# Kernel tuning notes

Hardware: AMD Instinct MI355X
Metric: run time of the kernel (lower is better)

Reference implementation:

```python
import jax, jax.numpy as jnp
import numpy as np

DIM = 768
HEADS = 12

def setup_inputs() -> dict:
    key = jax.random.key(0)
    ks = jax.random.split(key, 5)
    x = jax.random.normal(ks[0], (8, 1024, DIM), dtype=jnp.float32)
    s = 1.0 / np.sqrt(DIM)
    W_qkv = jax.random.normal(ks[1], (DIM, 3 * DIM), dtype=jnp.float32) * s
    b_qkv = jax.random.normal(ks[2], (3 * DIM,), dtype=jnp.float32) * 0.01
    W_proj = jax.random.normal(ks[3], (DIM, DIM), dtype=jnp.float32) * s
    b_proj = jax.random.normal(ks[4], (DIM,), dtype=jnp.float32) * 0.01
    return {"x": x, "W_qkv": W_qkv, "b_qkv": b_qkv, "W_proj": W_proj, "b_proj": b_proj}

def reference(x, W_qkv, b_qkv, W_proj, b_proj):
    B, T, D = x.shape
    H = HEADS
    hd = D // H
    scale = hd ** -0.5
    qkv = x @ W_qkv + b_qkv                      # [B,T,3D]
    qkv = qkv.reshape(B, T, 3, H, hd)
    q, k, v = jnp.moveaxis(qkv, 2, 0)            # each [B,T,H,hd]
    q = jnp.transpose(q, (0, 2, 1, 3))           # [B,H,T,hd]
    k = jnp.transpose(k, (0, 2, 1, 3))
    v = jnp.transpose(v, (0, 2, 1, 3))
    attn = jnp.einsum('bhqd,bhkd->bhqk', q, k) * scale
    attn = jax.nn.softmax(attn, axis=-1)
    y = jnp.einsum('bhqk,bhkd->bhqd', attn, v)   # [B,H,T,hd]
    y = jnp.transpose(y, (0, 2, 1, 3)).reshape(B, T, D)
    return y @ W_proj + b_proj
```

## Files before the change

### kernel.cpp

```cpp
#include <hip/hip_runtime.h>

typedef unsigned short u16;
typedef __attribute__((ext_vector_type(8))) short short8;
typedef __attribute__((ext_vector_type(4))) short short4v;
typedef __attribute__((ext_vector_type(2))) int int2v;
typedef __attribute__((ext_vector_type(4))) float f32x4;

#define DIM   768
#define HEADS 12
#define HD    64
#define BATCH 8
#define SEQ   1024
#define MTOK  (BATCH*SEQ)
#define NQKV  (3*DIM)
#define KP    72
#define EPAD  66
#define PSZ   ((size_t)BATCH*HEADS*SEQ*HD)
#define SCQ   0.1803368801f

__device__ __forceinline__ u16 f2bf(float f) {
  unsigned x = __float_as_uint(f);
  x += 0x7fffu + ((x >> 16) & 1u);
  return (u16)(x >> 16);
}

__device__ __forceinline__ void gload16(const u16* g, u16* l) {
  __builtin_amdgcn_global_load_lds(
      (const __attribute__((address_space(1))) unsigned int*)g,
      (__attribute__((address_space(3))) unsigned int*)l, 16, 0, 0);
}

#define XBLK 6144
#define QTBLK 1728
__global__ void cvt_all_k(const float* __restrict__ x,
                          const float* __restrict__ Wqkv,
                          const float* __restrict__ Wproj,
                          u16* __restrict__ xb, u16* __restrict__ wqkvt,
                          u16* __restrict__ wprojt) {
  __shared__ u16 tile[32][33];
  const int blk = blockIdx.x;
  if (blk < XBLK) {
    const int i = blk * 256 + threadIdx.x;
    float4 f = ((const float4*)x)[i];
    short4v o;
    o.x = (short)f2bf(f.x); o.y = (short)f2bf(f.y);
    o.z = (short)f2bf(f.z); o.w = (short)f2bf(f.w);
    ((short4v*)xb)[i] = o;
    return;
  }
  const float* in; u16* out; int K, N, n0, k0;
  if (blk < XBLK + QTBLK) {
    const int t = blk - XBLK;
    in = Wqkv; out = wqkvt; K = DIM; N = NQKV;
    n0 = (t % (NQKV / 32)) * 32; k0 = (t / (NQKV / 32)) * 32;
  } else {
    const int t = blk - XBLK - QTBLK;
    in = Wproj; out = wprojt; K = DIM; N = DIM;
    n0 = (t % (DIM / 32)) * 32; k0 = (t / (DIM / 32)) * 32;
  }
  const int tx = threadIdx.x & 31, ty = threadIdx.x >> 5;
  #pragma unroll
  for (int i = 0; i < 32; i += 8)
    tile[ty + i][tx] = f2bf(in[(size_t)(k0 + ty + i) * N + n0 + tx]);
  __syncthreads();
  #pragma unroll
  for (int i = 0; i < 32; i += 8)
    out[(size_t)(n0 + ty + i) * K + k0 + tx] = tile[tx][ty + i];
}

__global__ __launch_bounds__(256)
void gemm_qkv(const u16* __restrict__ A, const u16* __restrict__ Bt,
              const float* __restrict__ bias, u16* __restrict__ qkv) {
  __shared__ __align__(16) u16 smem[8 * 128 * 32];
  const int w = threadIdx.x >> 6, lane = threadIdx.x & 63;
  const int l15 = lane & 15, quad = lane >> 4;
  const int b_ = blockIdx.x;
  const int xcd = b_ & 7, j = b_ >> 3;
  const int m0 = ((j & 7) * 8 + xcd) * 128;
  const int n0 = (j >> 3) * 128;
  const int wm = (w >> 1) * 64, wn = (w & 1) * 64;

  f32x4 acc[4][4] = {};

  const int ar = threadIdx.x >> 2, ak = (threadIdx.x & 3) * 8;
  const u16* ga = A  + (size_t)(m0 + ar) * DIM + ak;
  const u16* gb = Bt + (size_t)(n0 + ar) * DIM + ak;
  const int lo = threadIdx.x * 8;

  auto qstage = [&](int c, int k0) {
    u16* base = smem + c * 16384;
    #pragma unroll
    for (int t = 0; t < 2; ++t) {
      gload16(ga + (size_t)t * 64 * DIM + k0,      base + lo + t * 2048);
      gload16(ga + (size_t)t * 64 * DIM + k0 + 32, base + 4096  + lo + t * 2048);
      gload16(gb + (size_t)t * 64 * DIM + k0,      base + 8192  + lo + t * 2048);
      gload16(gb + (size_t)t * 64 * DIM + k0 + 32, base + 12288 + lo + t * 2048);
    }
  };

  qstage(0, 0);

  #pragma unroll
  for (int it = 0; it < 12; ++it) {
    const int cur = it & 1;
    if (it < 11) qstage(cur ^ 1, (it + 1) * 64);
    if (it < 11) asm volatile("s_waitcnt vmcnt(8)" ::: "memory");
    else         asm volatile("s_waitcnt vmcnt(0)" ::: "memory");
    __builtin_amdgcn_s_barrier();

    const u16* hb = smem + cur * 16384;
    short8 af[4][2], bfr[4][2];
    #pragma unroll
    for (int kh = 0; kh < 2; ++kh) {
      const u16* lAh = hb + kh * 4096;
      const u16* lBh = hb + 8192 + kh * 4096;
      #pragma unroll
      for (int mt = 0; mt < 4; ++mt)
        af[mt][kh] = *(const short8*)&lAh[(wm + mt * 16 + l15) * 32 + quad * 8];
      #pragma unroll
      for (int nt = 0; nt < 4; ++nt)
        bfr[nt][kh] = *(const short8*)&lBh[(wn + nt * 16 + l15) * 32 + quad * 8];
    }

    asm volatile("s_waitcnt lgkmcnt(0)" ::: "memory");
    __builtin_amdgcn_s_barrier();

    #pragma unroll
    for (int kh = 0; kh < 2; ++kh)
      #pragma unroll
      for (int mt = 0; mt < 4; ++mt)
        #pragma unroll
        for (int nt = 0; nt < 4; ++nt)
          acc[mt][nt] = __builtin_amdgcn_mfma_f32_16x16x32_bf16(af[mt][kh], bfr[nt][kh], acc[mt][nt], 0, 0, 0);
  }

  const int bb = m0 >> 10;
  const int tb0 = (m0 & 1023) + wm;
  const int nh = n0 + wn;
  const int part = nh / DIM, idx = nh - part * DIM;
  const int h = idx >> 6;

  float bnl[4];
  #pragma unroll
  for (int nt = 0; nt < 4; ++nt) bnl[nt] = bias[nh + nt * 16 + l15];

  if (part < 2) {
    u16* dstbase = qkv + part * PSZ + ((size_t)(bb * HEADS + h) * SEQ + tb0) * HD;
    const float qsc = (part == 0) ? SCQ : 1.0f;
    const int erow = lane >> 3, ec8 = (lane & 7) * 8;
    #pragma unroll
    for (int mt = 0; mt < 4; ++mt) {
      u16* ep = smem + w * (16 * EPAD) + (mt & 1) * (4 * 16 * EPAD);
      #pragma unroll
      for (int nt = 0; nt < 4; ++nt)
        #pragma unroll
        for (int r = 0; r < 4; ++r)
          ep[(quad * 4 + r) * EPAD + nt * 16 + l15] = f2bf((acc[mt][nt][r] + bnl[nt]) * qsc);
      #pragma unroll
      for (int j2 = 0; j2 < 2; ++j2) {
        const int trow = j2 * 8 + erow;
        short8 vrow = *(const short8*)&ep[trow * EPAD + ec8];
        *(short8*)(dstbase + (size_t)(mt * 16 + trow) * HD + ec8) = vrow;
      }
    }
  } else {
    u16* vrow0 = qkv + 2 * PSZ + (size_t)(bb * HEADS + h) * HD * SEQ;
    #pragma unroll
    for (int nt = 0; nt < 4; ++nt) {
      const int d = nt * 16 + l15;
      u16* trow = vrow0 + (size_t)d * SEQ + tb0 + quad * 4;
      #pragma unroll
      for (int mt = 0; mt < 4; ++mt) {
        short4v pv;
        pv.x = (short)f2bf(acc[mt][nt][0] + bnl[nt]);
        pv.y = (short)f2bf(acc[mt][nt][1] + bnl[nt]);
        pv.z = (short)f2bf(acc[mt][nt][2] + bnl[nt]);
        pv.w = (short)f2bf(acc[mt][nt][3] + bnl[nt]);
        *(short4v*)(trow + mt * 16) = pv;
      }
    }
  }
}

__global__ __launch_bounds__(256)
void gemm_proj(const u16* __restrict__ A, const u16* __restrict__ Bt,
               const float* __restrict__ bias, float* __restrict__ outF) {
  __shared__ __align__(16) u16 smem[8 * 128 * 32];
  const int w = threadIdx.x >> 6, lane = threadIdx.x & 63;
  const int l15 = lane & 15, quad = lane >> 4;
  const int b_ = blockIdx.x;
  const int xcd = b_ & 7, j = b_ >> 3;
  const int m0 = ((j & 7) * 8 + xcd) * 128;
  const int n0 = (j >> 3) * 128;
  const int wm = (w >> 1) * 64, wn = (w & 1) * 64;

  f32x4 acc[4][4] = {};

  const int ar = threadIdx.x >> 2, ak = (threadIdx.x & 3) * 8;
  const u16* ga = A  + (size_t)(m0 + ar) * DIM + ak;
  const u16* gb = Bt + (size_t)(n0 + ar) * DIM + ak;
  const int lo = threadIdx.x * 8;

  auto pstage = [&](int c, int k0) {
    u16* base = smem + c * 16384;
    #pragma unroll
    for (int t = 0; t < 2; ++t) {
      gload16(ga + (size_t)t * 64 * DIM + k0,      base + lo + t * 2048);
      gload16(ga + (size_t)t * 64 * DIM + k0 + 32, base + 4096  + lo + t * 2048);
      gload16(gb + (size_t)t * 64 * DIM + k0,      base + 8192  + lo + t * 2048);
      gload16(gb + (size_t)t * 64 * DIM + k0 + 32, base + 12288 + lo + t * 2048);
    }
  };

  pstage(0, 0);
  __syncthreads();

  #pragma unroll
  for (int it = 0; it < 12; ++it) {
    const int cur = it & 1;
    if (it < 11) pstage(cur ^ 1, (it + 1) * 64);
    const u16* hb = smem + cur * 16384;
    #pragma unroll
    for (int kh = 0; kh < 2; ++kh) {
      const u16* lAh = hb + kh * 4096;
      const u16* lBh = hb + 8192 + kh * 4096;
      short8 af[4], bfr[4];
      #pragma unroll
      for (int mt = 0; mt < 4; ++mt)
        af[mt] = *(const short8*)&lAh[(wm + mt * 16 + l15) * 32 + quad * 8];
      #pragma unroll
      for (int nt = 0; nt < 4; ++nt)
        bfr[nt] = *(const short8*)&lBh[(wn + nt * 16 + l15) * 32 + quad * 8];
      #pragma unroll
      for (int mt = 0; mt < 4; ++mt)
        #pragma unroll
        for (int nt = 0; nt < 4; ++nt)
          acc[mt][nt] = __builtin_amdgcn_mfma_f32_16x16x32_bf16(af[mt], bfr[nt], acc[mt][nt], 0, 0, 0);
    }
    __syncthreads();
  }

  #pragma unroll
  for (int nt = 0; nt < 4; ++nt) {
    const int n = n0 + wn + nt * 16 + l15;
    const float bn = bias[n];
    #pragma unroll
    for (int mt = 0; mt < 4; ++mt)
      #pragma unroll
      for (int r = 0; r < 4; ++r) {
        const int m = m0 + wm + mt * 16 + quad * 4 + r;
        outF[(size_t)m * DIM + n] = acc[mt][nt][r] + bn;
      }
  }
}

__global__ __launch_bounds__(512, 4)
void attn_k(const u16* __restrict__ qb, const u16* __restrict__ kb,
            const u16* __restrict__ vtb, u16* __restrict__ yb) {
  const int bh = blockIdx.x, qt = blockIdx.y;
  const int tid = threadIdx.x;
  const int w = tid >> 6, lane = tid & 63;
  const int l15 = lane & 15, quad = lane >> 4;
  const int rg = w & 3;
  const int kh = w >> 2;
  const int nt0 = kh * 2;

  __shared__ __align__(16) u16 smem[27648];
  u16* lK  = smem;
  u16* lV  = smem + 4608;
  u16* lPq = smem + 9216 + rg * 2304;
  u16* stg = smem + 18432 + rg * 2304;
  float* fo = (float*)smem;

  const u16* qrow = qb + ((size_t)bh * SEQ + qt * 128 + rg * 32 + l15) * HD;
  short8 aq[2][2];
  #pragma unroll
  for (int qg = 0; qg < 2; ++qg) {
    aq[qg][0] = *(const short8*)(qrow + (size_t)qg * 16 * HD + quad * 8);
    aq[qg][1] = *(const short8*)(qrow + (size_t)qg * 16 * HD + 32 + quad * 8);
  }

  f32x4 o[2][4] = {};
  f32x4 sum[2] = {};

  const u16* kcbase = kb + (size_t)bh * SEQ * HD;
  const u16* vbase  = vtb + (size_t)bh * HD * SEQ;

  const int srow = tid >> 3, scol = tid & 7;
  const int sofs = srow * KP + scol * 8;
  const u16* kg = kcbase + tid * 8;
  const u16* vg = vbase + (size_t)srow * SEQ + scol * 8;

  short8 pk = *(const short8*)kg;
  short8 pv = *(const short8*)vg;

  short8 ones;
  #pragma unroll
  for (int i = 0; i < 8; ++i) ones[i] = (short)0x3f80;

  for (int kc = 0; kc < 16; ++kc) {
    *(short8*)&lK[sofs] = pk;
    *(short8*)&lV[sofs] = pv;
    __syncthreads();

    const int kn = (kc < 15) ? kc + 1 : 15;
    pk = *(const short8*)(kg + (size_t)kn * 64 * HD);
    pv = *(const short8*)(vg + kn * 64);

    short8 akf[2][2];
    #pragma unroll
    for (int i = 0; i < 2; ++i) {
      const int key = (nt0 + i) * 16 + l15;
      akf[i][0] = *(const short8*)&lK[key * KP + quad * 8];
      akf[i][1] = *(const short8*)&lK[key * KP + 32 + quad * 8];
    }

    #pragma unroll
    for (int qg = 0; qg < 2; ++qg) {
      f32x4 s0 = {}, s1 = {};
      __builtin_amdgcn_s_setprio(1);
      s0 = __builtin_amdgcn_mfma_f32_16x16x32_bf16(akf[0][0], aq[qg][0], s0, 0, 0, 0);
      s0 = __builtin_amdgcn_mfma_f32_16x16x32_bf16(akf[0][1], aq[qg][1], s0, 0, 0, 0);
      s1 = __builtin_amdgcn_mfma_f32_16x16x32_bf16(akf[1][0], aq[qg][0], s1, 0, 0, 0);
      s1 = __builtin_amdgcn_mfma_f32_16x16x32_bf16(akf[1][1], aq[qg][1], s1, 0, 0, 0);
      __builtin_amdgcn_s_setprio(0);
      #pragma unroll
      for (int i = 0; i < 2; ++i) {
        const f32x4 s = i ? s1 : s0;
        float p0 = __builtin_amdgcn_exp2f(s[0]);
        float p1 = __builtin_amdgcn_exp2f(s[1]);
        float p2 = __builtin_amdgcn_exp2f(s[2]);
        float p3 = __builtin_amdgcn_exp2f(s[3]);
        int2v pkk;
        pkk.x = (int)__builtin_amdgcn_perm(__float_as_uint(p1), __float_as_uint(p0), 0x07060302u);
        pkk.y = (int)__builtin_amdgcn_perm(__float_as_uint(p3), __float_as_uint(p2), 0x07060302u);
        *(int2v*)&lPq[(qg * 16 + l15) * KP + (nt0 + i) * 16 + quad * 4] = pkk;
      }
    }

    short8 bv[4];
    #pragma unroll
    for (int ntd = 0; ntd < 4; ++ntd)
      bv[ntd] = *(const short8*)&lV[(ntd * 16 + l15) * KP + kh * 32 + quad * 8];

    #pragma unroll
    for (int qg = 0; qg < 2; ++qg) {
      const short8 ap = *(const short8*)&lPq[(qg * 16 + l15) * KP + kh * 32 + quad * 8];
      __builtin_amdgcn_s_setprio(1);
      #pragma unroll
      for (int ntd = 0; ntd < 4; ++ntd)
        o[qg][ntd] = __builtin_amdgcn_mfma_f32_16x16x32_bf16(ap, bv[ntd], o[qg][ntd], 0, 0, 0);
      sum[qg] = __builtin_amdgcn_mfma_f32_16x16x32_bf16(ap, ones, sum[qg], 0, 0, 0);
      __builtin_amdgcn_s_setprio(0);
    }
    __syncthreads();
  }

  if (kh == 1) {
    #pragma unroll
    for (int qg = 0; qg < 2; ++qg)
      #pragma unroll
      for (int r = 0; r < 4; ++r) {
        const int row = rg * 32 + qg * 16 + quad * 4 + r;
        #pragma unroll
        for (int ntd = 0; ntd < 4; ++ntd)
          fo[row * 68 + ntd * 16 + l15] = o[qg][ntd][r];
        if (l15 == 0) fo[row * 68 + 64] = sum[qg][r];
      }
  }
  __syncthreads();

  if (kh == 0) {
    const int b = bh / HEADS, h = bh % HEADS;
    #pragma unroll
    for (int qg = 0; qg < 2; ++qg)
      #pragma unroll
      for (int r = 0; r < 4; ++r) {
        const int lrow = qg * 16 + quad * 4 + r;
        const int row = rg * 32 + lrow;
        const float s = sum[qg][r] + fo[row * 68 + 64];
        const float inv = 1.0f / s;
        #pragma unroll
        for (int ntd = 0; ntd < 4; ++ntd) {
          const float v = (o[qg][ntd][r] + fo[row * 68 + ntd * 16 + l15]) * inv;
          stg[lrow * KP + ntd * 16 + l15] = f2bf(v);
        }
      }
    u16* dst = yb + ((size_t)b * SEQ + qt * 128 + rg * 32) * DIM + h * HD;
    const int erow = lane >> 3, ec8 = (lane & 7) * 8;
    #pragma unroll
    for (int j = 0; j < 4; ++j) {
      const int trow = j * 8 + erow;
      short8 vrow = *(const short8*)&stg[trow * KP + ec8];
      *(short8*)(dst + (size_t)trow * DIM + ec8) = vrow;
    }
  }
}

extern "C" void kernel_launch(void* const* d_in, const int* in_sizes, int n_in,
                              void* d_out, int out_size, void* d_ws, size_t ws_size,
                              hipStream_t stream) {
  const float* x     = (const float*)d_in[0];
  const float* Wqkv  = (const float*)d_in[1];
  const float* bqkv  = (const float*)d_in[2];
  const float* Wproj = (const float*)d_in[3];
  const float* bproj = (const float*)d_in[4];
  float* out = (float*)d_out;

  u16* xb     = (u16*)d_ws;
  u16* wqkvt  = xb + (size_t)MTOK * DIM;
  u16* wprojt = wqkvt + (size_t)NQKV * DIM;
  u16* qkv_b  = wprojt + (size_t)DIM * DIM;
  u16* y_b    = qkv_b + 3 * PSZ;

  cvt_all_k<<<XBLK + QTBLK + (DIM / 32) * (DIM / 32), 256, 0, stream>>>(
      x, Wqkv, Wproj, xb, wqkvt, wprojt);

  gemm_qkv<<<1152, 256, 0, stream>>>(xb, wqkvt, bqkv, qkv_b);

  attn_k<<<dim3(BATCH * HEADS, SEQ / 128), 512, 0, stream>>>(
      qkv_b, qkv_b + PSZ, qkv_b + 2 * PSZ, y_b);

  gemm_proj<<<384, 256, 0, stream>>>(y_b, wprojt, bproj, out);
}
```

Before: 180.4 us.

## Double-buffer K/V tiles via direct global-to-LDS loads with XOR swizzle

Replaces the register-prefetch then LDS-store staging of K and V tiles in the attention kernel with direct global-to-LDS loads (gload16) into two LDS buffers. The next chunk's loads are issued while the current one is computed, and synchronisation uses explicit vmcnt waits and raw barriers. The padded row stride of 72 is replaced by an unpadded 64-element stride with an XOR chunk swizzle to avoid bank conflicts. The aim is to hide global load latency and cut VGPR traffic and LDS padding, at the cost of more delicate wait-count logic that relies on a gload16 helper defined elsewhere.

```diff
diff --git a/kernel.cpp b/kernel.cpp
--- a/kernel.cpp
+++ b/kernel.cpp
@@ -265,11 +265,9 @@
   const int kh = w >> 2;
   const int nt0 = kh * 2;
 
-  __shared__ __align__(16) u16 smem[27648];
-  u16* lK  = smem;
-  u16* lV  = smem + 4608;
-  u16* lPq = smem + 9216 + rg * 2304;
-  u16* stg = smem + 18432 + rg * 2304;
+  __shared__ __align__(16) u16 smem[26624];
+  u16* lPq = smem + 16384 + rg * 2304;
+  u16* stg = smem + 17408 + rg * 2304;
   float* fo = (float*)smem;
 
   const u16* qrow = qb + ((size_t)bh * SEQ + qt * 128 + rg * 32 + l15) * HD;
@@ -286,33 +284,40 @@
   const u16* kcbase = kb + (size_t)bh * SEQ * HD;
   const u16* vbase  = vtb + (size_t)bh * HD * SEQ;
 
-  const int srow = tid >> 3, scol = tid & 7;
-  const int sofs = srow * KP + scol * 8;
-  const u16* kg = kcbase + tid * 8;
-  const u16* vg = vbase + (size_t)srow * SEQ + scol * 8;
-
-  short8 pk = *(const short8*)kg;
-  short8 pv = *(const short8*)vg;
+  const int srow = tid >> 3;
+  const int schunk = (tid & 7) ^ (srow & 7);
+  const u16* kgs = kcbase + (size_t)srow * HD + schunk * 8;
+  const u16* vgs = vbase + (size_t)srow * SEQ + schunk * 8;
+  const int dst = tid * 8;
+
+  auto stage = [&](int c, int kc) {
+    gload16(kgs + kc * 4096, smem + c * 8192 + dst);
+    gload16(vgs + kc * 64,   smem + c * 8192 + 4096 + dst);
+  };
 
   short8 ones;
   #pragma unroll
   for (int i = 0; i < 8; ++i) ones[i] = (short)0x3f80;
 
+  stage(0, 0);
+
   for (int kc = 0; kc < 16; ++kc) {
-    *(short8*)&lK[sofs] = pk;
-    *(short8*)&lV[sofs] = pv;
-    __syncthreads();
-
-    const int kn = (kc < 15) ? kc + 1 : 15;
-    pk = *(const short8*)(kg + (size_t)kn * 64 * HD);
-    pv = *(const short8*)(vg + kn * 64);
+    const int cur = kc & 1;
+    if (kc < 15) stage(cur ^ 1, kc + 1);
+    if (kc < 15) asm volatile("s_waitcnt vmcnt(2)" ::: "memory");
+    else         asm volatile("s_waitcnt vmcnt(0)" ::: "memory");
+    __builtin_amdgcn_s_barrier();
+
+    const u16* lK = smem + cur * 8192;
+    const u16* lV = lK + 4096;
+    const int sx = l15 & 7;
 
     short8 akf[2][2];
     #pragma unroll
     for (int i = 0; i < 2; ++i) {
       const int key = (nt0 + i) * 16 + l15;
-      akf[i][0] = *(const short8*)&lK[key * KP + quad * 8];
-      akf[i][1] = *(const short8*)&lK[key * KP + 32 + quad * 8];
+      akf[i][0] = *(const short8*)&lK[key * 64 + ((quad ^ sx) * 8)];
+      akf[i][1] = *(const short8*)&lK[key * 64 + (((4 + quad) ^ sx) * 8)];
     }
 
     #pragma unroll
@@ -341,7 +346,7 @@
     short8 bv[4];
     #pragma unroll
     for (int ntd = 0; ntd < 4; ++ntd)
-      bv[ntd] = *(const short8*)&lV[(ntd * 16 + l15) * KP + kh * 32 + quad * 8];
+      bv[ntd] = *(const short8*)&lV[(ntd * 16 + l15) * 64 + (((kh * 4 + quad) ^ sx) * 8)];
 
     #pragma unroll
     for (int qg = 0; qg < 2; ++qg) {
@@ -353,7 +358,9 @@
       sum[qg] = __builtin_amdgcn_mfma_f32_16x16x32_bf16(ap, ones, sum[qg], 0, 0, 0);
       __builtin_amdgcn_s_setprio(0);
     }
-    __syncthreads();
+
+    asm volatile("s_waitcnt lgkmcnt(0)" ::: "memory");
+    __builtin_amdgcn_s_barrier();
   }
 
   if (kh == 1) {
@@ -386,13 +393,13 @@
           stg[lrow * KP + ntd * 16 + l15] = f2bf(v);
         }
       }
-    u16* dst = yb + ((size_t)b * SEQ + qt * 128 + rg * 32) * DIM + h * HD;
+    u16* dst2 = yb + ((size_t)b * SEQ + qt * 128 + rg * 32) * DIM + h * HD;
     const int erow = lane >> 3, ec8 = (lane & 7) * 8;
     #pragma unroll
     for (int j = 0; j < 4; ++j) {
       const int trow = j * 8 + erow;
       short8 vrow = *(const short8*)&stg[trow * KP + ec8];
-      *(short8*)(dst + (size_t)trow * DIM + ec8) = vrow;
+      *(short8*)(dst2 + (size_t)trow * DIM + ec8) = vrow;
     }
   }
 }
```

Result: faster. 173.4 us (-3.9%).
